# Kernel tuning notes

Hardware: AMD Instinct MI355X
Metric: run time of the kernel (lower is better)

Reference implementation:

```python
import jax, jax.numpy as jnp
import numpy as np

DIM = 2048
N_HEADS = 32
N_KV_HEADS = 8
HEAD_DIM = 64
REPEATS = N_HEADS // N_KV_HEADS
SCALE = HEAD_DIM ** -0.5
L = 2048
B = 1


def rotary_matrix(context_len, d):
    # Dense (L, d, d) RoPE rotation matrix, exactly as get_rotary_matrix1.
    pos = jnp.arange(1, context_len + 1, dtype=jnp.float32)[:, None]
    i = jnp.arange(d // 2)
    theta = 10000.0 ** (-2.0 * i.astype(jnp.float32) / d)
    m_theta = pos * theta  # (L, d/2)
    cos_v, sin_v = jnp.cos(m_theta), jnp.sin(m_theta)
    R = jnp.zeros((context_len, d, d), dtype=jnp.float32)
    R = R.at[:, 2 * i, 2 * i].set(cos_v)
    R = R.at[:, 2 * i, 2 * i + 1].set(-sin_v)
    R = R.at[:, 2 * i + 1, 2 * i].set(sin_v)
    R = R.at[:, 2 * i + 1, 2 * i + 1].set(cos_v)
    return R


def causal_mask(context_len):
    idx = jnp.arange(context_len)
    return (idx[:, None] < idx[None, :]).astype(jnp.float32) * -1e9


def setup_inputs() -> dict:
    key = jax.random.key(0)
    ks = jax.random.split(key, 5)
    x = jax.random.normal(ks[0], (B, L, DIM), dtype=jnp.float32)
    mask = causal_mask(L)
    wq_w = jax.random.normal(ks[1], (N_HEADS * HEAD_DIM, DIM), dtype=jnp.float32) * 0.02
    wk_w = jax.random.normal(ks[2], (N_KV_HEADS * HEAD_DIM, DIM), dtype=jnp.float32) * 0.02
    wv_w = jax.random.normal(ks[3], (N_KV_HEADS * HEAD_DIM, DIM), dtype=jnp.float32) * 0.02
    wo_w = jax.random.normal(ks[4], (DIM, N_HEADS * HEAD_DIM), dtype=jnp.float32) * 0.02
    return {"x": x, "mask": mask, "wq_w": wq_w, "wk_w": wk_w, "wv_w": wv_w, "wo_w": wo_w}


def reference(x, mask, wq_w, wk_w, wv_w, wo_w):
    Bx, Lx, D = x.shape
    # projections (torch Linear: y = x @ W.T)
    q = jnp.einsum('bld,od->blo', x, wq_w).reshape(Bx, Lx, N_HEADS, HEAD_DIM).transpose(0, 2, 1, 3)
    k = jnp.einsum('bld,od->blo', x, wk_w).reshape(Bx, Lx, N_KV_HEADS, HEAD_DIM).transpose(0, 2, 1, 3)
    v = jnp.einsum('bld,od->blo', x, wv_w).reshape(Bx, Lx, N_KV_HEADS, HEAD_DIM).transpose(0, 2, 1, 3)
    # GQA repeat of kv heads (interleaved, matching concat-unsqueeze-reshape)
    k = jnp.repeat(k, REPEATS, axis=1)
    v = jnp.repeat(v, REPEATS, axis=1)
    # dense-matrix RoPE on q and (repeated) k
    R = rotary_matrix(Lx, HEAD_DIM)
    q = jnp.einsum('bhlj,lij->bhli', q, R)
    k = jnp.einsum('bhlj,lij->bhli', k, R)
    scores = jnp.einsum('bhld,bhmd->bhlm', q, k) * SCALE + mask
    attn = jax.nn.softmax(scores.astype(jnp.float32), axis=-1)
    out = jnp.einsum('bhlm,bhmd->bhld', attn, v)
    out = out.transpose(0, 2, 1, 3).reshape(Bx, Lx, N_HEADS * HEAD_DIM)
    out = jnp.einsum('blo,do->bld', out, wo_w)
    return out, k, v
```

## Files before the change

### kernel.cpp

```cpp
#include <hip/hip_runtime.h>

typedef __bf16 bf16;
typedef __bf16 bf16x8 __attribute__((ext_vector_type(8)));
typedef float floatx4 __attribute__((ext_vector_type(4)));
typedef float floatx16 __attribute__((ext_vector_type(16)));
typedef unsigned int uint;

#define MFMA16(a, b, c) __builtin_amdgcn_mfma_f32_16x16x32_bf16((a), (b), (c), 0, 0, 0)
#define MFMA32(a, b, c) __builtin_amdgcn_mfma_f32_32x32x16_bf16((a), (b), (c), 0, 0, 0)

__device__ __forceinline__ void gl2lds16(const bf16* g, bf16* l) {
  __builtin_amdgcn_global_load_lds(
      (const __attribute__((address_space(1))) void*)g,
      (__attribute__((address_space(3))) void*)l, 16, 0, 0);
}
__device__ __forceinline__ void wait_vm0() { __builtin_amdgcn_s_waitcnt(0x0f70); }

__device__ __forceinline__ void cvt8(const float* __restrict__ s,
                                     bf16* __restrict__ d, int i8) {
  const float4 a = ((const float4*)s)[i8 * 2];
  const float4 b = ((const float4*)s)[i8 * 2 + 1];
  bf16x8 o;
  o[0] = (bf16)a.x; o[1] = (bf16)a.y; o[2] = (bf16)a.z; o[3] = (bf16)a.w;
  o[4] = (bf16)b.x; o[5] = (bf16)b.y; o[6] = (bf16)b.z; o[7] = (bf16)b.w;
  *(bf16x8*)(d + i8 * 8) = o;
}

__global__ __launch_bounds__(256) void convert_kernel(
    const float* __restrict__ x, const float* __restrict__ wq,
    const float* __restrict__ wk, const float* __restrict__ wv,
    const float* __restrict__ wo, bf16* __restrict__ xb,
    bf16* __restrict__ wqb, bf16* __restrict__ wkb, bf16* __restrict__ wvb,
    bf16* __restrict__ wob) {
  const int g = blockIdx.x * 256 + threadIdx.x;
  if (g < 524288) cvt8(x, xb, g);
  else if (g < 1048576) cvt8(wq, wqb, g - 524288);
  else if (g < 1179648) cvt8(wk, wkb, g - 1048576);
  else if (g < 1310720) cvt8(wv, wvb, g - 1179648);
  else cvt8(wo, wob, g - 1310720);
}

template <typename OutT>
__device__ __forceinline__ void gemm_tile_body(
    const bf16* __restrict__ A, int lda,
    const bf16* __restrict__ B, int ldb,
    OutT* __restrict__ C, int ldc, int K,
    bf16* As, bf16* Bs) {
  const int t = threadIdx.x;
  const int w = t >> 6, lane = t & 63;
  const int l15 = lane & 15, qd = lane >> 4;
  const int wr = w >> 1, wc = w & 1;

  floatx4 acc[4][4];
#pragma unroll
  for (int i = 0; i < 4; ++i)
#pragma unroll
    for (int j = 0; j < 4; ++j) acc[i][j] = (floatx4){0.f, 0.f, 0.f, 0.f};

  const int mt0 = w, mt1 = w + 4;
  const int kseg = qd * 8;
  const bf16* ga0 = A + (mt0 * 16 + l15) * lda + kseg;
  const bf16* ga1 = A + (mt1 * 16 + l15) * lda + kseg;
  const bf16* gb0 = B + (mt0 * 16 + l15) * ldb + kseg;
  const bf16* gb1 = B + (mt1 * 16 + l15) * ldb + kseg;
  bf16* lA0 = As + mt0 * 512 + lane * 8;
  bf16* lA1 = As + mt1 * 512 + lane * 8;
  bf16* lB0 = Bs + mt0 * 512 + lane * 8;
  bf16* lB1 = Bs + mt1 * 512 + lane * 8;

  for (int k0 = 0; k0 < K; k0 += 32) {
    gl2lds16(ga0 + k0, lA0);
    gl2lds16(ga1 + k0, lA1);
    gl2lds16(gb0 + k0, lB0);
    gl2lds16(gb1 + k0, lB1);
    wait_vm0();
    __syncthreads();

    bf16x8 a[4], b[4];
#pragma unroll
    for (int i = 0; i < 4; ++i)
      a[i] = *(const bf16x8*)(As + (wr * 4 + i) * 512 + lane * 8);
#pragma unroll
    for (int j = 0; j < 4; ++j)
      b[j] = *(const bf16x8*)(Bs + (wc * 4 + j) * 512 + lane * 8);
#pragma unroll
    for (int i = 0; i < 4; ++i)
#pragma unroll
      for (int j = 0; j < 4; ++j) acc[i][j] = MFMA16(a[i], b[j], acc[i][j]);
    __syncthreads();
  }

#pragma unroll
  for (int i = 0; i < 4; ++i)
#pragma unroll
    for (int j = 0; j < 4; ++j) {
      const int row = wr * 64 + i * 16 + qd * 4;
      const int col = wc * 64 + j * 16 + l15;
#pragma unroll
      for (int r = 0; r < 4; ++r)
        C[(row + r) * ldc + col] = (OutT)acc[i][j][r];
    }
}

__global__ __launch_bounds__(256) void gemm_qkv(
    const bf16* __restrict__ x, const bf16* __restrict__ wq,
    const bf16* __restrict__ wk, const bf16* __restrict__ wv,
    bf16* __restrict__ Qws, bf16* __restrict__ Kws, bf16* __restrict__ Vws) {
  __shared__ bf16 As[4096], Bs[4096];
  const int m0 = blockIdx.y * 128;
  const int nb = blockIdx.x;
  const bf16* B;
  bf16* C;
  int ldc;
  if (nb < 16) {
    B = wq + nb * 128 * 2048;
    C = Qws + m0 * 2048 + nb * 128;
    ldc = 2048;
  } else if (nb < 20) {
    B = wk + (nb - 16) * 128 * 2048;
    C = Kws + m0 * 512 + (nb - 16) * 128;
    ldc = 512;
  } else {
    B = wv + (nb - 20) * 128 * 2048;
    C = Vws + m0 * 512 + (nb - 20) * 128;
    ldc = 512;
  }
  gemm_tile_body<bf16>(x + m0 * 2048, 2048, B, 2048, C, ldc, 2048, As, Bs);
}

__global__ __launch_bounds__(256) void gemm_o(
    const bf16* __restrict__ Ows, const bf16* __restrict__ wo,
    float* __restrict__ out) {
  __shared__ bf16 As[4096], Bs[4096];
  const int m0 = blockIdx.y * 128, n0 = blockIdx.x * 128;
  gemm_tile_body<float>(Ows + m0 * 2048, 2048, wo + n0 * 2048, 2048,
                        out + m0 * 2048 + n0, 2048, 2048, As, Bs);
}

__global__ __launch_bounds__(256) void rope_repeat_kernel(
    bf16* __restrict__ Qws, bf16* __restrict__ Kws, bf16* __restrict__ Kh,
    const bf16* __restrict__ Vws, bf16* __restrict__ Vt,
    float* __restrict__ kout, float* __restrict__ vout) {
  const int gid = blockIdx.x * 256 + threadIdx.x;
  const float NEG_LOG2_10000_D32 = -0.4152410118609203f;
  if (gid < 2097152) {
    const int l = gid >> 10, pr = gid & 1023, a = pr & 31;
    bf16* p = Qws + l * 2048 + pr * 2;
    const float x0 = (float)p[0], x1 = (float)p[1];
    const float ang = (float)(l + 1) * exp2f(NEG_LOG2_10000_D32 * (float)a);
    float s, c;
    __sincosf(ang, &s, &c);
    p[0] = (bf16)(c * x0 - s * x1);
    p[1] = (bf16)(s * x0 + c * x1);
  } else if (gid < 2097152 + 524288) {
    const int g = gid - 2097152;
    const int l = g >> 8, pr = g & 255, a = pr & 31, kvh = pr >> 5;
    bf16* p = Kws + l * 512 + pr * 2;
    const float x0 = (float)p[0], x1 = (float)p[1];
    const float ang = (float)(l + 1) * exp2f(NEG_LOG2_10000_D32 * (float)a);
    float s, c;
    __sincosf(ang, &s, &c);
    const float y0 = c * x0 - s * x1;
    const float y1 = s * x0 + c * x1;
    p[0] = (bf16)y0;
    p[1] = (bf16)y1;
    bf16* kp = Kh + (kvh * 2048 + l) * 64 + a * 2;
    kp[0] = (bf16)y0;
    kp[1] = (bf16)y1;
#pragma unroll
    for (int rep = 0; rep < 4; ++rep) {
      float* o = kout + (((kvh * 4 + rep) * 2048 + l) * 64 + a * 2);
      o[0] = y0;
      o[1] = y1;
    }
  } else if (gid < 2097152 + 524288 + 131072) {
    const int c = gid - (2097152 + 524288);
    const int l = c >> 6, seg = c & 63, kvh = seg >> 3;
    const bf16x8 v = *(const bf16x8*)(Vws + l * 512 + seg * 8);
    float4 f0, f1;
    f0.x = (float)v[0]; f0.y = (float)v[1]; f0.z = (float)v[2]; f0.w = (float)v[3];
    f1.x = (float)v[4]; f1.y = (float)v[5]; f1.z = (float)v[6]; f1.w = (float)v[7];
#pragma unroll
    for (int rep = 0; rep < 4; ++rep) {
      float* o = vout + (((kvh * 4 + rep) * 2048 + l) * 64 + (seg & 7) * 8);
      *(float4*)o = f0;
      *(float4*)(o + 4) = f1;
    }
  } else {
    const int c = gid - (2097152 + 524288 + 131072);
    const int kvh = c >> 14, r2 = c & 16383, dseg = r2 >> 11, l = r2 & 2047;
    const int d0 = dseg * 8;
    const bf16x8 v = *(const bf16x8*)(Vws + l * 512 + kvh * 64 + d0);
#pragma unroll
    for (int jj = 0; jj < 8; ++jj)
      Vt[kvh * 131072 + (d0 + jj) * 2048 + l] = v[jj];
  }
}

__global__ __launch_bounds__(256) void flash_kernel(
    const bf16* __restrict__ Qws, const bf16* __restrict__ Kh,
    const bf16* __restrict__ Vt, bf16* __restrict__ Ows,
    float* __restrict__ Opart, float* __restrict__ ML) {
  __shared__ bf16 KVs[2][2][4096];
  __shared__ bf16 Osh[128 * 66];

  const int h = blockIdx.y;
  const int bx = blockIdx.x;
  int qt, seg, kts, kte;
  if (bx < 8) {
    qt = bx; seg = -1; kts = 0; kte = 2 * qt + 2;
  } else {
    const int i = bx - 8;
    qt = 8 + (i >> 1);
    seg = i & 1;
    const int half = qt + 1;
    kts = seg * half;
    kte = kts + half;
  }
  const int kh = h >> 2;
  const int q0 = qt * 128;
  const int t = threadIdx.x, w = t >> 6, lane = t & 63;
  const int l31 = lane & 31, hf = lane >> 5;
  const int qw = q0 + w * 32;

  bf16x8 qf[4];
  {
    const bf16* qrow = Qws + (qw + l31) * 2048 + h * 64 + hf * 8;
#pragma unroll
    for (int c = 0; c < 4; ++c) qf[c] = *(const bf16x8*)(qrow + c * 16);
  }

  floatx16 o[2] = {};
  float mrun = -3e38f, lrun = 0.f;

  const int s0 = w, s1 = w + 4;
  const bf16* gK0 = Kh + kh * 131072 + ((s0 >> 2) * 32 + l31) * 64 + (s0 & 3) * 16 + hf * 8;
  const bf16* gK1 = Kh + kh * 131072 + ((s1 >> 2) * 32 + l31) * 64 + (s1 & 3) * 16 + hf * 8;
  const bf16* gV0 = Vt + kh * 131072 + ((s0 >> 2) * 32 + l31) * 2048 + (s0 & 3) * 16 + hf * 8;
  const bf16* gV1 = Vt + kh * 131072 + ((s1 >> 2) * 32 + l31) * 2048 + (s1 & 3) * 16 + hf * 8;

  {
    const int nb = kts & 1;
    gl2lds16(gK0 + kts * 4096, &KVs[nb][0][s0 * 512 + lane * 8]);
    gl2lds16(gK1 + kts * 4096, &KVs[nb][0][s1 * 512 + lane * 8]);
    gl2lds16(gV0 + kts * 64, &KVs[nb][1][s0 * 512 + lane * 8]);
    gl2lds16(gV1 + kts * 64, &KVs[nb][1][s1 * 512 + lane * 8]);
  }

  const float C = 0.1803368801f;
  for (int kt = kts; kt < kte; ++kt) {
    wait_vm0();
    __syncthreads();
    if (kt + 1 < kte) {
      const int nb = (kt + 1) & 1;
      const int koff = (kt + 1) * 4096, voff = (kt + 1) * 64;
      gl2lds16(gK0 + koff, &KVs[nb][0][s0 * 512 + lane * 8]);
      gl2lds16(gK1 + koff, &KVs[nb][0][s1 * 512 + lane * 8]);
      gl2lds16(gV0 + voff, &KVs[nb][1][s0 * 512 + lane * 8]);
      gl2lds16(gV1 + voff, &KVs[nb][1][s1 * 512 + lane * 8]);
    }
    const int kt64 = kt * 64;
    if (kt64 > qw + 31) continue;
    const bf16* Kb = &KVs[kt & 1][0][0];
    const bf16* Vb = &KVs[kt & 1][1][0];

    floatx16 st[2];
    __builtin_amdgcn_s_setprio(1);
#pragma unroll
    for (int tt = 0; tt < 2; ++tt) {
      floatx16 z = {};
#pragma unroll
      for (int c = 0; c < 4; ++c) {
        const bf16x8 kf = *(const bf16x8*)(Kb + (tt * 4 + c) * 512 + lane * 8);
        z = MFMA32(kf, qf[c], z);
      }
      st[tt] = z;
    }
    __builtin_amdgcn_s_setprio(0);
    if (kt64 + 64 > qw) {
      const int myq = qw + l31;
#pragma unroll
      for (int tt = 0; tt < 2; ++tt)
#pragma unroll
        for (int r = 0; r < 16; ++r) {
          const int key = kt64 + tt * 32 + (r & 3) + 8 * (r >> 2) + 4 * hf;
          if (key > myq) st[tt][r] = -1e30f;
        }
    }
    float ma = -3e38f, mb = -3e38f, mc = -3e38f, md = -3e38f;
#pragma unroll
    for (int tt = 0; tt < 2; ++tt)
#pragma unroll
      for (int r = 0; r < 16; r += 4) {
        ma = fmaxf(ma, st[tt][r + 0]);
        mb = fmaxf(mb, st[tt][r + 1]);
        mc = fmaxf(mc, st[tt][r + 2]);
        md = fmaxf(md, st[tt][r + 3]);
      }
    float mx = fmaxf(fmaxf(ma, mb), fmaxf(mc, md));
    mx = fmaxf(mx, __shfl_xor(mx, 32));
    const bool defer = __all((mx - mrun) * C <= 8.f);
    if (!defer) {
      const float mn = fmaxf(mrun, mx);
      const float al = __builtin_amdgcn_exp2f((mrun - mn) * C);
      lrun *= al;
#pragma unroll
      for (int n = 0; n < 2; ++n)
#pragma unroll
        for (int r = 0; r < 16; ++r) o[n][r] *= al;
      mrun = mn;
    }
    float ra = 0.f, rb = 0.f, rc = 0.f, rd = 0.f;
#pragma unroll
    for (int tt = 0; tt < 2; ++tt)
#pragma unroll
      for (int r = 0; r < 16; r += 4) {
        const float p0 = __builtin_amdgcn_exp2f((st[tt][r + 0] - mrun) * C);
        const float p1 = __builtin_amdgcn_exp2f((st[tt][r + 1] - mrun) * C);
        const float p2 = __builtin_amdgcn_exp2f((st[tt][r + 2] - mrun) * C);
        const float p3 = __builtin_amdgcn_exp2f((st[tt][r + 3] - mrun) * C);
        st[tt][r + 0] = p0; ra += p0;
        st[tt][r + 1] = p1; rb += p1;
        st[tt][r + 2] = p2; rc += p2;
        st[tt][r + 3] = p3; rd += p3;
      }
    float rs = (ra + rb) + (rc + rd);
    rs += __shfl_xor(rs, 32);
    lrun += rs;

    uint pk[2][4][2];
#pragma unroll
    for (int tt = 0; tt < 2; ++tt)
#pragma unroll
      for (int g = 0; g < 4; ++g)
#pragma unroll
        for (int p = 0; p < 2; ++p) {
          union { bf16 h2[2]; uint u; } cv;
          cv.h2[0] = (bf16)st[tt][4 * g + 2 * p];
          cv.h2[1] = (bf16)st[tt][4 * g + 2 * p + 1];
          pk[tt][g][p] = cv.u;
        }
    uint own_[2][2][2], rv[2][2][2];
#pragma unroll
    for (int tt = 0; tt < 2; ++tt)
#pragma unroll
      for (int gam = 0; gam < 2; ++gam)
#pragma unroll
        for (int p = 0; p < 2; ++p) {
          own_[tt][gam][p] = hf ? pk[tt][2 * gam + 1][p] : pk[tt][2 * gam][p];
          const uint snd = hf ? pk[tt][2 * gam][p] : pk[tt][2 * gam + 1][p];
          rv[tt][gam][p] = (uint)__shfl_xor((int)snd, 32);
        }
    __builtin_amdgcn_s_setprio(1);
#pragma unroll
    for (int c = 0; c < 4; ++c) {
      const int tt = c >> 1, gam = c & 1;
      union { uint u[4]; bf16x8 v; } pf;
      pf.u[0] = hf ? rv[tt][gam][0] : own_[tt][gam][0];
      pf.u[1] = hf ? rv[tt][gam][1] : own_[tt][gam][1];
      pf.u[2] = hf ? own_[tt][gam][0] : rv[tt][gam][0];
      pf.u[3] = hf ? own_[tt][gam][1] : rv[tt][gam][1];
#pragma unroll
      for (int n = 0; n < 2; ++n)
        o[n] = MFMA32(*(const bf16x8*)(Vb + (n * 4 + c) * 512 + lane * 8),
                      pf.v, o[n]);
    }
    __builtin_amdgcn_s_setprio(0);
  }

  if (seg < 0) {
    const float inv = 1.f / lrun;
#pragma unroll
    for (int n = 0; n < 2; ++n)
#pragma unroll
      for (int r = 0; r < 16; ++r) {
        const int dl = n * 32 + (r & 3) + 8 * (r >> 2) + 4 * hf;
        Osh[(w * 32 + l31) * 66 + dl] = (bf16)(o[n][r] * inv);
      }
    __syncthreads();
#pragma unroll
    for (int i = 0; i < 4; ++i) {
      const int row = (t >> 3) + i * 32;
      const int col = (t & 7) * 8;
      const bf16x8 vv = *(const bf16x8*)&Osh[row * 66 + col];
      *(bf16x8*)&Ows[(q0 + row) * 2048 + h * 64 + col] = vv;
    }
  } else {
    const int idx = (h * 8 + (qt - 8)) * 2 + seg;
    float* Op = Opart + idx * 8192;
#pragma unroll
    for (int n = 0; n < 2; ++n)
#pragma unroll
      for (int r = 0; r < 16; ++r) {
        const int dl = n * 32 + (r & 3) + 8 * (r >> 2) + 4 * hf;
        Op[dl * 128 + w * 32 + l31] = o[n][r];
      }
    if (hf == 0) {
      ML[idx * 256 + w * 32 + l31] = mrun;
      ML[idx * 256 + 128 + w * 32 + l31] = lrun;
    }
  }
}

__global__ __launch_bounds__(256) void combine_kernel(
    const float* __restrict__ Opart, const float* __restrict__ ML,
    bf16* __restrict__ Ows) {
  __shared__ bf16 Osh[128 * 66];
  const int b = blockIdx.x;
  const int h = b >> 3, qt = (b & 7) + 8;
  const int q0 = qt * 128;
  const int t = threadIdx.x;
  const int row = t & 127, dh = t >> 7;
  const int i0 = (h * 8 + (qt - 8)) * 2;
  const float C = 0.1803368801f;
  const float m0 = ML[i0 * 256 + row], l0 = ML[i0 * 256 + 128 + row];
  const float m1 = ML[(i0 + 1) * 256 + row], l1 = ML[(i0 + 1) * 256 + 128 + row];
  const float m = fmaxf(m0, m1);
  const float w0 = __builtin_amdgcn_exp2f((m0 - m) * C);
  const float w1 = __builtin_amdgcn_exp2f((m1 - m) * C);
  const float inv = 1.f / (l0 * w0 + l1 * w1);
  const float* P0 = Opart + i0 * 8192;
  const float* P1 = Opart + (i0 + 1) * 8192;
#pragma unroll
  for (int j = 0; j < 32; ++j) {
    const int d = dh * 32 + j;
    const float v = (P0[d * 128 + row] * w0 + P1[d * 128 + row] * w1) * inv;
    Osh[row * 66 + d] = (bf16)v;
  }
  __syncthreads();
#pragma unroll
  for (int i = 0; i < 4; ++i) {
    const int r2 = (t >> 3) + i * 32;
    const int col = (t & 7) * 8;
    const bf16x8 vv = *(const bf16x8*)&Osh[r2 * 66 + col];
    *(bf16x8*)&Ows[(q0 + r2) * 2048 + h * 64 + col] = vv;
  }
}

extern "C" void kernel_launch(void* const* d_in, const int* in_sizes, int n_in,
                              void* d_out, int out_size, void* d_ws,
                              size_t ws_size, hipStream_t stream) {
  const float* x = (const float*)d_in[0];
  const float* wq = (const float*)d_in[2];
  const float* wk = (const float*)d_in[3];
  const float* wv = (const float*)d_in[4];
  const float* wo = (const float*)d_in[5];

  float* out = (float*)d_out;
  float* kout = out + 4194304;
  float* vout = out + 8388608;

  bf16* ws = (bf16*)d_ws;
  bf16* xb = ws;
  bf16* wqb = xb + 4194304;
  bf16* wkb = wqb + 4194304;
  bf16* wvb = wkb + 1048576;
  bf16* wob = wvb + 1048576;
  bf16* Qws = wob + 4194304;
  bf16* Kws = Qws + 4194304;
  bf16* Vws = Kws + 1048576;
  bf16* Vt = Vws + 1048576;
  bf16* Ows = Vt + 1048576;
  bf16* Kh = Ows + 4194304;
  float* Opart = out;
  float* MLf = (float*)Kws;

  convert_kernel<<<dim3(7168), dim3(256), 0, stream>>>(x, wq, wk, wv, wo, xb,
                                                       wqb, wkb, wvb, wob);
  gemm_qkv<<<dim3(24, 16), dim3(256), 0, stream>>>(xb, wqb, wkb, wvb, Qws, Kws,
                                                   Vws);
  rope_repeat_kernel<<<dim3(11264), dim3(256), 0, stream>>>(Qws, Kws, Kh, Vws,
                                                            Vt, kout, vout);
  flash_kernel<<<dim3(24, 32), dim3(256), 0, stream>>>(Qws, Kh, Vt, Ows, Opart,
                                                       MLf);
  combine_kernel<<<dim3(256), dim3(256), 0, stream>>>(Opart, MLf, Ows);
  gemm_o<<<dim3(16, 16), dim3(256), 0, stream>>>(Ows, wob, out);
}
```

Before: 307.7 us.

## Multi-buffer GEMM LDS tiles with 3-deep async prefetch pipeline

Replaces the single-buffered load/wait/compute loop in the shared GEMM tile body with a 4-slot LDS ring buffer. Three k-tiles are prefetched ahead using partial vmcnt waits, so global-to-LDS loads overlap with MFMA work, and only one barrier is needed per iteration. LDS use per block rises fourfold to 64 KB, which may lower occupancy. The write-after-read safety of the ring depends on the single barrier placed before each new stage is issued.

```diff
diff --git a/kernel.cpp b/kernel.cpp
--- a/kernel.cpp
+++ b/kernel.cpp
@@ -15,6 +15,8 @@
       (__attribute__((address_space(3))) void*)l, 16, 0, 0);
 }
 __device__ __forceinline__ void wait_vm0() { __builtin_amdgcn_s_waitcnt(0x0f70); }
+__device__ __forceinline__ void wait_vm4() { __builtin_amdgcn_s_waitcnt(0x0f74); }
+__device__ __forceinline__ void wait_vm8() { __builtin_amdgcn_s_waitcnt(0x0f78); }
 
 __device__ __forceinline__ void cvt8(const float* __restrict__ s,
                                      bf16* __restrict__ d, int i8) {
@@ -63,32 +65,50 @@
   const bf16* ga1 = A + (mt1 * 16 + l15) * lda + kseg;
   const bf16* gb0 = B + (mt0 * 16 + l15) * ldb + kseg;
   const bf16* gb1 = B + (mt1 * 16 + l15) * ldb + kseg;
-  bf16* lA0 = As + mt0 * 512 + lane * 8;
-  bf16* lA1 = As + mt1 * 512 + lane * 8;
-  bf16* lB0 = Bs + mt0 * 512 + lane * 8;
-  bf16* lB1 = Bs + mt1 * 512 + lane * 8;
-
-  for (int k0 = 0; k0 < K; k0 += 32) {
-    gl2lds16(ga0 + k0, lA0);
-    gl2lds16(ga1 + k0, lA1);
-    gl2lds16(gb0 + k0, lB0);
-    gl2lds16(gb1 + k0, lB1);
-    wait_vm0();
-    __syncthreads();
-
+  const int lofs0 = mt0 * 512 + lane * 8;
+  const int lofs1 = mt1 * 512 + lane * 8;
+
+  const int NT = K >> 5;
+#define STAGE(kt_, b_)                                  \
+  do {                                                  \
+    const int k0_ = (kt_) * 32;                         \
+    bf16* As_ = As + (b_) * 4096;                       \
+    bf16* Bs_ = Bs + (b_) * 4096;                       \
+    gl2lds16(ga0 + k0_, As_ + lofs0);                   \
+    gl2lds16(ga1 + k0_, As_ + lofs1);                   \
+    gl2lds16(gb0 + k0_, Bs_ + lofs0);                   \
+    gl2lds16(gb1 + k0_, Bs_ + lofs1);                   \
+  } while (0)
+
+  STAGE(0, 0);
+  STAGE(1, 1);
+  STAGE(2, 2);
+
+  for (int kt = 0; kt < NT; ++kt) {
+    const int rem = NT - 1 - kt;
+    if (rem >= 2) wait_vm8();
+    else if (rem == 1) wait_vm4();
+    else wait_vm0();
+    __builtin_amdgcn_sched_barrier(0);
+    __builtin_amdgcn_s_barrier();
+    __builtin_amdgcn_sched_barrier(0);
+    if (kt + 3 < NT) STAGE(kt + 3, (kt + 3) & 3);
+
+    const bf16* Ab = As + (kt & 3) * 4096;
+    const bf16* Bb = Bs + (kt & 3) * 4096;
     bf16x8 a[4], b[4];
 #pragma unroll
     for (int i = 0; i < 4; ++i)
-      a[i] = *(const bf16x8*)(As + (wr * 4 + i) * 512 + lane * 8);
+      a[i] = *(const bf16x8*)(Ab + (wr * 4 + i) * 512 + lane * 8);
 #pragma unroll
     for (int j = 0; j < 4; ++j)
-      b[j] = *(const bf16x8*)(Bs + (wc * 4 + j) * 512 + lane * 8);
+      b[j] = *(const bf16x8*)(Bb + (wc * 4 + j) * 512 + lane * 8);
 #pragma unroll
     for (int i = 0; i < 4; ++i)
 #pragma unroll
       for (int j = 0; j < 4; ++j) acc[i][j] = MFMA16(a[i], b[j], acc[i][j]);
-    __syncthreads();
-  }
+  }
+#undef STAGE
 
 #pragma unroll
   for (int i = 0; i < 4; ++i)
@@ -106,7 +126,7 @@
     const bf16* __restrict__ x, const bf16* __restrict__ wq,
     const bf16* __restrict__ wk, const bf16* __restrict__ wv,
     bf16* __restrict__ Qws, bf16* __restrict__ Kws, bf16* __restrict__ Vws) {
-  __shared__ bf16 As[4096], Bs[4096];
+  __shared__ bf16 As[16384], Bs[16384];
   const int m0 = blockIdx.y * 128;
   const int nb = blockIdx.x;
   const bf16* B;
@@ -131,7 +151,7 @@
 __global__ __launch_bounds__(256) void gemm_o(
     const bf16* __restrict__ Ows, const bf16* __restrict__ wo,
     float* __restrict__ out) {
-  __shared__ bf16 As[4096], Bs[4096];
+  __shared__ bf16 As[16384], Bs[16384];
   const int m0 = blockIdx.y * 128, n0 = blockIdx.x * 128;
   gemm_tile_body<float>(Ows + m0 * 2048, 2048, wo + n0 * 2048, 2048,
                         out + m0 * 2048 + n0, 2048, 2048, As, Bs);
```

New measurement: 303.2 us. Within noise of the previous version (-1.4%).

## Double-buffer GEMM K-tiles with 64-row tiles and K=64 steps

Applied to the files above, without the earlier changes.

Rewrites the shared GEMM body so that global-to-LDS loads for the next K tile go into a second buffer while the MFMAs run on the current one. It also halves the M tile to 64 rows, which doubles the grid for both the QKV and output projections to fill more CUs, and widens the K step to 64. The aim is to hide load latency and cut the barrier count per K. In exchange it uses more LDS per block and does less reuse of each loaded B tile.

```diff
diff --git a/kernel.cpp b/kernel.cpp
--- a/kernel.cpp
+++ b/kernel.cpp
@@ -41,60 +41,86 @@
 }
 
 template <typename OutT>
-__device__ __forceinline__ void gemm_tile_body(
+__device__ __forceinline__ void gemm_tile_body64(
     const bf16* __restrict__ A, int lda,
     const bf16* __restrict__ B, int ldb,
     OutT* __restrict__ C, int ldc, int K,
-    bf16* As, bf16* Bs) {
+    bf16* S) {
   const int t = threadIdx.x;
   const int w = t >> 6, lane = t & 63;
   const int l15 = lane & 15, qd = lane >> 4;
   const int wr = w >> 1, wc = w & 1;
 
-  floatx4 acc[4][4];
-#pragma unroll
-  for (int i = 0; i < 4; ++i)
+  floatx4 acc[2][4];
+#pragma unroll
+  for (int i = 0; i < 2; ++i)
 #pragma unroll
     for (int j = 0; j < 4; ++j) acc[i][j] = (floatx4){0.f, 0.f, 0.f, 0.f};
 
-  const int mt0 = w, mt1 = w + 4;
-  const int kseg = qd * 8;
-  const bf16* ga0 = A + (mt0 * 16 + l15) * lda + kseg;
-  const bf16* ga1 = A + (mt1 * 16 + l15) * lda + kseg;
-  const bf16* gb0 = B + (mt0 * 16 + l15) * ldb + kseg;
-  const bf16* gb1 = B + (mt1 * 16 + l15) * ldb + kseg;
-  bf16* lA0 = As + mt0 * 512 + lane * 8;
-  bf16* lA1 = As + mt1 * 512 + lane * 8;
-  bf16* lB0 = Bs + mt0 * 512 + lane * 8;
-  bf16* lB1 = Bs + mt1 * 512 + lane * 8;
-
-  for (int k0 = 0; k0 < K; k0 += 32) {
-    gl2lds16(ga0 + k0, lA0);
-    gl2lds16(ga1 + k0, lA1);
-    gl2lds16(gb0 + k0, lB0);
-    gl2lds16(gb1 + k0, lB1);
+  const bf16* gb[6];
+  int lo[6];
+#pragma unroll
+  for (int i = 0; i < 6; ++i) {
+    const int u = w + 4 * i;
+    lo[i] = u * 512 + lane * 8;
+    if (u < 8) {
+      gb[i] = A + ((u >> 1) * 16 + l15) * lda + (u & 1) * 32 + qd * 8;
+    } else {
+      const int v = u - 8;
+      gb[i] = B + ((v >> 1) * 16 + l15) * ldb + (v & 1) * 32 + qd * 8;
+    }
+  }
+
+#define STG64(kt_, buf_)                                            \
+  {                                                                 \
+    bf16* d_ = S + (buf_) * 12288;                                  \
+    _Pragma("unroll")                                               \
+    for (int i_ = 0; i_ < 6; ++i_)                                  \
+      gl2lds16(gb[i_] + (kt_) * 64, d_ + lo[i_]);                   \
+  }
+
+  const int NT = K >> 6;
+  STG64(0, 0);
+  wait_vm0();
+  __syncthreads();
+  int cur = 0;
+  for (int kt = 0; kt < NT; ++kt) {
+    if (kt + 1 < NT) STG64(kt + 1, cur ^ 1);
+    const bf16* Ab = S + cur * 12288;
+    const bf16* Bb = Ab + 4096;
+    bf16x8 a[2][2], b[4][2];
+#pragma unroll
+    for (int i = 0; i < 2; ++i)
+#pragma unroll
+      for (int kk = 0; kk < 2; ++kk)
+        a[i][kk] =
+            *(const bf16x8*)(Ab + ((wr * 2 + i) * 2 + kk) * 512 + lane * 8);
+#pragma unroll
+    for (int j = 0; j < 4; ++j)
+#pragma unroll
+      for (int kk = 0; kk < 2; ++kk)
+        b[j][kk] =
+            *(const bf16x8*)(Bb + ((wc * 4 + j) * 2 + kk) * 512 + lane * 8);
+#pragma unroll
+    for (int kk = 0; kk < 2; ++kk)
+#pragma unroll
+      for (int i = 0; i < 2; ++i)
+#pragma unroll
+        for (int j = 0; j < 4; ++j)
+          acc[i][j] = MFMA16(a[i][kk], b[j][kk], acc[i][j]);
     wait_vm0();
-    __syncthreads();
-
-    bf16x8 a[4], b[4];
-#pragma unroll
-    for (int i = 0; i < 4; ++i)
-      a[i] = *(const bf16x8*)(As + (wr * 4 + i) * 512 + lane * 8);
-#pragma unroll
-    for (int j = 0; j < 4; ++j)
-      b[j] = *(const bf16x8*)(Bs + (wc * 4 + j) * 512 + lane * 8);
-#pragma unroll
-    for (int i = 0; i < 4; ++i)
-#pragma unroll
-      for (int j = 0; j < 4; ++j) acc[i][j] = MFMA16(a[i], b[j], acc[i][j]);
-    __syncthreads();
-  }
-
-#pragma unroll
-  for (int i = 0; i < 4; ++i)
+    __builtin_amdgcn_sched_barrier(0);
+    __builtin_amdgcn_s_barrier();
+    __builtin_amdgcn_sched_barrier(0);
+    cur ^= 1;
+  }
+#undef STG64
+
+#pragma unroll
+  for (int i = 0; i < 2; ++i)
 #pragma unroll
     for (int j = 0; j < 4; ++j) {
-      const int row = wr * 64 + i * 16 + qd * 4;
+      const int row = wr * 32 + i * 16 + qd * 4;
       const int col = wc * 64 + j * 16 + l15;
 #pragma unroll
       for (int r = 0; r < 4; ++r)
@@ -106,8 +132,8 @@
     const bf16* __restrict__ x, const bf16* __restrict__ wq,
     const bf16* __restrict__ wk, const bf16* __restrict__ wv,
     bf16* __restrict__ Qws, bf16* __restrict__ Kws, bf16* __restrict__ Vws) {
-  __shared__ bf16 As[4096], Bs[4096];
-  const int m0 = blockIdx.y * 128;
+  __shared__ bf16 S[24576];
+  const int m0 = blockIdx.y * 64;
   const int nb = blockIdx.x;
   const bf16* B;
   bf16* C;
@@ -125,16 +151,16 @@
     C = Vws + m0 * 512 + (nb - 20) * 128;
     ldc = 512;
   }
-  gemm_tile_body<bf16>(x + m0 * 2048, 2048, B, 2048, C, ldc, 2048, As, Bs);
+  gemm_tile_body64<bf16>(x + m0 * 2048, 2048, B, 2048, C, ldc, 2048, S);
 }
 
 __global__ __launch_bounds__(256) void gemm_o(
     const bf16* __restrict__ Ows, const bf16* __restrict__ wo,
     float* __restrict__ out) {
-  __shared__ bf16 As[4096], Bs[4096];
-  const int m0 = blockIdx.y * 128, n0 = blockIdx.x * 128;
-  gemm_tile_body<float>(Ows + m0 * 2048, 2048, wo + n0 * 2048, 2048,
-                        out + m0 * 2048 + n0, 2048, 2048, As, Bs);
+  __shared__ bf16 S[24576];
+  const int m0 = blockIdx.y * 64, n0 = blockIdx.x * 128;
+  gemm_tile_body64<float>(Ows + m0 * 2048, 2048, wo + n0 * 2048, 2048,
+                          out + m0 * 2048 + n0, 2048, 2048, S);
 }
 
 __global__ __launch_bounds__(256) void rope_repeat_kernel(
@@ -467,12 +493,12 @@
 
   convert_kernel<<<dim3(7168), dim3(256), 0, stream>>>(x, wq, wk, wv, wo, xb,
                                                        wqb, wkb, wvb, wob);
-  gemm_qkv<<<dim3(24, 16), dim3(256), 0, stream>>>(xb, wqb, wkb, wvb, Qws, Kws,
+  gemm_qkv<<<dim3(24, 32), dim3(256), 0, stream>>>(xb, wqb, wkb, wvb, Qws, Kws,
                                                    Vws);
   rope_repeat_kernel<<<dim3(11264), dim3(256), 0, stream>>>(Qws, Kws, Kh, Vws,
                                                             Vt, kout, vout);
   flash_kernel<<<dim3(24, 32), dim3(256), 0, stream>>>(Qws, Kh, Vt, Ows, Opart,
                                                        MLf);
   combine_kernel<<<dim3(256), dim3(256), 0, stream>>>(Opart, MLf, Ows);
-  gemm_o<<<dim3(16, 16), dim3(256), 0, stream>>>(Ows, wob, out);
-}
+  gemm_o<<<dim3(16, 32), dim3(256), 0, stream>>>(Ows, wob, out);
+}
```

Measured after the change: 297.7 us. 1.03x faster.
